# Kernel tuning notes

Hardware: AMD Instinct MI355X
Metric: run time of the kernel (lower is better)

Reference implementation:

```python
import jax, jax.numpy as jnp
import numpy as np

N_NODES = 50000
N_EDGES = 400000
HID = 128
EPS_GEN = 1e-7  # GENConv message eps


def layernorm(x, w, b, eps=1e-5):
    mu = x.mean(-1, keepdims=True)
    var = x.var(-1, keepdims=True)
    return (x - mu) / jnp.sqrt(var + eps) * w + b


def segment_softmax(v, seg, n):
    # per-channel softmax over edges sharing the same destination node
    m = jax.ops.segment_max(v, seg, num_segments=n)
    e = jnp.exp(v - m[seg])
    s = jax.ops.segment_sum(e, seg, num_segments=n)
    return e / (s[seg] + 1e-16)


def genconv(x, src, dst, w1, b1, lnw, lnb, w2, b2, t):
    # GENConv(aggr='softmax', t learnable, mlp num_layers=2, norm='layer'), no edge_attr
    n = x.shape[0]
    msg = jax.nn.relu(x[src]) + EPS_GEN            # [E, H]
    alpha = segment_softmax(msg * t, dst, n)       # [E, H]
    aggr = jax.ops.segment_sum(msg * alpha, dst, num_segments=n)  # [N, H]
    h = x + aggr                                   # residual self term
    h = layernorm(h @ w1 + b1, lnw, lnb)           # Linear(H, 2H) + LayerNorm + ReLU
    return jax.nn.relu(h) @ w2 + b2                # Linear(2H, H)


def setup_inputs() -> dict:
    key = jax.random.key(0)
    ks = jax.random.split(key, 30)
    rn = lambda k, shape, s=0.02: jax.random.normal(k, shape, jnp.float32) * s
    inp = {}
    inp['x'] = jax.random.normal(ks[0], (N_NODES, 1024), jnp.float32)
    inp['edge_index'] = jax.random.randint(ks[1], (2, N_EDGES), 0, N_NODES, jnp.int64 if jax.config.jax_enable_x64 else jnp.int32)
    inp['fc_w'] = rn(ks[2], (1024, HID)); inp['fc_b'] = jnp.zeros((HID,), jnp.float32)
    inp['conv_w1'] = rn(ks[3], (3, HID, 2 * HID)); inp['conv_b1'] = jnp.zeros((3, 2 * HID), jnp.float32)
    inp['conv_lnw'] = jnp.ones((3, 2 * HID), jnp.float32); inp['conv_lnb'] = jnp.zeros((3, 2 * HID), jnp.float32)
    inp['conv_w2'] = rn(ks[4], (3, 2 * HID, HID)); inp['conv_b2'] = jnp.zeros((3, HID), jnp.float32)
    inp['conv_t'] = jnp.ones((3,), jnp.float32)
    inp['norm_w'] = jnp.ones((3, HID), jnp.float32); inp['norm_b'] = jnp.zeros((3, HID), jnp.float32)
    D = 4 * HID  # 512
    inp['phi_w'] = rn(ks[5], (D, D)); inp['phi_b'] = jnp.zeros((D,), jnp.float32)
    inp['attn_a_w'] = rn(ks[6], (D, D)); inp['attn_a_b'] = jnp.zeros((D,), jnp.float32)
    inp['attn_b_w'] = rn(ks[7], (D, D)); inp['attn_b_b'] = jnp.zeros((D,), jnp.float32)
    inp['attn_c_w'] = rn(ks[8], (D, 1)); inp['attn_c_b'] = jnp.zeros((1,), jnp.float32)
    inp['rho_w'] = rn(ks[9], (D, D)); inp['rho_b'] = jnp.zeros((D,), jnp.float32)
    inp['cls_w'] = rn(ks[10], (D, 4)); inp['cls_b'] = jnp.zeros((4,), jnp.float32)
    return inp


def reference(x, edge_index, fc_w, fc_b, conv_w1, conv_b1, conv_lnw, conv_lnb,
              conv_w2, conv_b2, conv_t, norm_w, norm_b, phi_w, phi_b,
              attn_a_w, attn_a_b, attn_b_w, attn_b_b, attn_c_w, attn_c_b,
              rho_w, rho_b, cls_w, cls_b):
    src, dst = edge_index[0], edge_index[1]
    # fc (dropout = identity in eval)
    x = jax.nn.relu(x @ fc_w + fc_b)               # [N, 128]
    x_ = x
    # layers[0].conv only (no norm/act/residual)
    x = genconv(x, src, dst, conv_w1[0], conv_b1[0], conv_lnw[0], conv_lnb[0],
                conv_w2[0], conv_b2[0], conv_t[0])
    x_ = jnp.concatenate([x_, x], axis=1)
    # DeepGCNLayer block='res': h = act(norm(conv(x))); x = x + h
    for i in (1, 2):
        h = genconv(x, src, dst, conv_w1[i], conv_b1[i], conv_lnw[i], conv_lnb[i],
                    conv_w2[i], conv_b2[i], conv_t[i])
        h = jax.nn.relu(layernorm(h, norm_w[i], norm_b[i]))
        x = x + h
        x_ = jnp.concatenate([x_, x], axis=1)
    h = jax.nn.relu(x_ @ phi_w + phi_b)            # path_phi, [N, 512]
    a = jnp.tanh(h @ attn_a_w + attn_a_b)
    b = jax.nn.sigmoid(h @ attn_b_w + attn_b_b)
    A = (a * b) @ attn_c_w + attn_c_b              # [N, 1]
    A = jax.nn.softmax(A.T, axis=1)                # [1, N]
    hp = A @ h                                     # [1, 512] attention pooling
    hp = jax.nn.relu(hp @ rho_w + rho_b)[0]        # squeeze -> [512]
    logits = (hp @ cls_w + cls_b)[None, :]         # [1, 4]
    return logits
```

## Files before the change

### kernel.cpp

```cpp
#include <hip/hip_runtime.h>
#include <hip/hip_bf16.h>
#include <math.h>

typedef __bf16 bf16_t;
typedef __attribute__((ext_vector_type(8))) __bf16 bf16x8;
typedef __attribute__((ext_vector_type(2))) __bf16 bf16x2;
typedef __attribute__((ext_vector_type(4))) float f32x4;

__device__ __forceinline__ void gld_lds16(const void* g, void* s) {
    __builtin_amdgcn_global_load_lds(
        (__attribute__((address_space(1))) unsigned int*)g,
        (__attribute__((address_space(3))) unsigned int*)s,
        16, 0, 0);
}

__device__ __forceinline__ int2 sw_decode(int orig, int nwg, int NT) {
    int q = nwg >> 3, r = nwg & 7, xcd = orig & 7, idx = orig >> 3;
    int wg = (xcd < r ? xcd * (q + 1) : r * (q + 1) + (xcd - r) * q) + idx;
    int bx = wg / NT, by = wg - bx * NT;
    return make_int2(bx, by);
}

__global__ __launch_bounds__(256) void k_tconv(const float* __restrict__ in, bf16_t* __restrict__ out,
                                               int R, int C, int rs, int ro)
{
    __shared__ float tile[32][33];
    int bc = blockIdx.x * 32;
    int br = blockIdx.y * 32;
    int tx = threadIdx.x & 31, ty = threadIdx.x >> 5;
    #pragma unroll
    for (int i = 0; i < 32; i += 8) {
        int r = br + ty + i, c = bc + tx;
        tile[ty + i][tx] = (r < R && c < C) ? in[(long)r * C + c] : 0.f;
    }
    __syncthreads();
    #pragma unroll
    for (int i = 0; i < 32; i += 8) {
        int c = bc + ty + i, r = br + tx;
        if (c < C && r < R) out[((long)c * rs + ro) * R + r] = (bf16_t)tile[tx][ty + i];
    }
}

__global__ __launch_bounds__(256) void k_bcat(const float* __restrict__ ab, const float* __restrict__ bb,
                                              float* __restrict__ bc)
{
    int i = blockIdx.x * 256 + threadIdx.x;
    if (i < 512) { bc[2 * i] = ab[i]; bc[2 * i + 1] = bb[i]; }
}

__global__ __launch_bounds__(256) void k_deg(const int* __restrict__ dst, int* __restrict__ deg, int E)
{
    int e = blockIdx.x * 256 + threadIdx.x;
    if (e < E) atomicAdd(&deg[dst[e]], 1);
}

__global__ __launch_bounds__(1024) void k_scan_a(const int* __restrict__ deg, int* __restrict__ loc,
                                                 int* __restrict__ bsum, int n)
{
    __shared__ int wsum[16];
    int t = threadIdx.x, lane = t & 63, wid = t >> 6;
    int idx = blockIdx.x * 1024 + t;
    int v = (idx < n) ? deg[idx] : 0;
    int x = v;
    #pragma unroll
    for (int d = 1; d < 64; d <<= 1) { int o = __shfl_up(x, d); if (lane >= d) x += o; }
    if (lane == 63) wsum[wid] = x;
    __syncthreads();
    if (wid == 0 && lane < 16) {
        int y = wsum[lane];
        #pragma unroll
        for (int d = 1; d < 16; d <<= 1) { int o = __shfl_up(y, d); if (lane >= d) y += o; }
        wsum[lane] = y;
    }
    __syncthreads();
    int wbase = (wid == 0) ? 0 : wsum[wid - 1];
    if (idx < n) loc[idx] = wbase + x - v;
    if (t == 1023) bsum[blockIdx.x] = wsum[15];
}

__global__ __launch_bounds__(64) void k_scan_b(const int* __restrict__ bsum, int nb,
                                               int* __restrict__ boff, int* __restrict__ off_n)
{
    int lane = threadIdx.x;
    int base = 0;
    for (int c = 0; c < nb; c += 64) {
        int i = c + lane;
        int v = (i < nb) ? bsum[i] : 0;
        int x = v;
        #pragma unroll
        for (int d = 1; d < 64; d <<= 1) { int o = __shfl_up(x, d); if (lane >= d) x += o; }
        if (i < nb) boff[i] = base + x - v;
        base += __shfl(x, 63);
    }
    if (lane == 0) *off_n = base;
}

__global__ __launch_bounds__(1024) void k_scan_c(const int* __restrict__ loc, const int* __restrict__ boff,
                                                 int* __restrict__ off, int* __restrict__ cursor, int n)
{
    int idx = blockIdx.x * 1024 + threadIdx.x;
    if (idx < n) { int v = loc[idx] + boff[blockIdx.x]; off[idx] = v; cursor[idx] = v; }
}

__global__ __launch_bounds__(256) void k_fill(const int* __restrict__ src, const int* __restrict__ dst,
                                              int* __restrict__ cursor, int* __restrict__ csr, int E)
{
    int e = blockIdx.x * 256 + threadIdx.x;
    if (e < E) {
        int d = dst[e];
        int pos = atomicAdd(&cursor[d], 1);
        csr[pos] = src[e];
    }
}

__global__ __launch_bounds__(256) void k_agg(const bf16_t* __restrict__ X,
                                             const int* __restrict__ off, const int* __restrict__ csr,
                                             bf16_t* __restrict__ haux,
                                             const float* __restrict__ tptr, int ti, int Nn)
{
    int w = (blockIdx.x * 256 + threadIdx.x) >> 6;
    if (w >= Nn) return;
    int lane = threadIdx.x & 63;
    float t = tptr[ti];
    int e0 = off[w], e1 = off[w + 1];
    float m0 = -__builtin_inff(), m1 = -__builtin_inff();
    float s0 = 0.f, s1 = 0.f, g0 = 0.f, g1 = 0.f;

    auto proc = [&](bf16x2 xv) {
        float msg0 = fmaxf((float)xv[0], 0.f) + 1e-7f;
        float msg1 = fmaxf((float)xv[1], 0.f) + 1e-7f;
        float v0 = msg0 * t, v1 = msg1 * t;
        if (v0 > m0) { float sc = __expf(m0 - v0); s0 *= sc; g0 *= sc; m0 = v0; }
        float p0 = __expf(v0 - m0); s0 += p0; g0 += msg0 * p0;
        if (v1 > m1) { float sc = __expf(m1 - v1); s1 *= sc; g1 *= sc; m1 = v1; }
        float p1 = __expf(v1 - m1); s1 += p1; g1 += msg1 * p1;
    };

    int e = e0;
    for (; e + 4 <= e1; e += 4) {
        int ia = csr[e], ib = csr[e + 1], ic = csr[e + 2], id = csr[e + 3];
        bf16x2 va = *(const bf16x2*)(X + (long)ia * 128 + lane * 2);
        bf16x2 vb = *(const bf16x2*)(X + (long)ib * 128 + lane * 2);
        bf16x2 vc = *(const bf16x2*)(X + (long)ic * 128 + lane * 2);
        bf16x2 vd = *(const bf16x2*)(X + (long)id * 128 + lane * 2);
        proc(va); proc(vb); proc(vc); proc(vd);
    }
    for (; e < e1; e++) {
        int s = csr[e];
        bf16x2 xv = *(const bf16x2*)(X + (long)s * 128 + lane * 2);
        proc(xv);
    }
    float a0 = g0 / (s0 + 1e-16f);
    float a1 = g1 / (s1 + 1e-16f);
    bf16x2 xr = *(const bf16x2*)(X + (long)w * 128 + lane * 2);
    bf16_t* outp = haux + (long)w * 128 + lane * 2;
    outp[0] = (bf16_t)((float)xr[0] + a0);
    outp[1] = (bf16_t)((float)xr[1] + a1);
}

template<int BM, int EPI>
__global__ __launch_bounds__((BM == 256) ? 512 : 256, 4)
void k_gemm1(const bf16_t* __restrict__ A, int lda,
             const bf16_t* __restrict__ BT,
             const float* __restrict__ bias,
             bf16_t* __restrict__ Cout, int ldc,
             int M, int K, int NT,
             const float* __restrict__ cw,
             float* __restrict__ sout)
{
    constexpr int THREADS = (BM == 256) ? 512 : 256;
    constexpr int ACH = BM * 8 / THREADS;
    constexpr int BCH = 128 * 8 / THREADS;
    __shared__ __align__(16) bf16_t lA[BM * 64];
    __shared__ __align__(16) bf16_t lB[128 * 64];
    int2 bxy = sw_decode(blockIdx.x, gridDim.x, NT);
    const int m0 = bxy.x * BM, n0 = bxy.y * 128;
    const int tid = threadIdx.x, lane = tid & 63, wid = tid >> 6;
    const int rbase = (wid >> 1) * 64, cbase = (wid & 1) * 64;
    const int lrow = lane & 15, kg = lane >> 4;
    const int uw = tid & ~63;

    f32x4 acc[4][4];
    #pragma unroll
    for (int m = 0; m < 4; m++)
        #pragma unroll
        for (int n = 0; n < 4; n++)
            #pragma unroll
            for (int r = 0; r < 4; r++) acc[m][n][r] = 0.f;

    auto stage = [&](int k0) {
        #pragma unroll
        for (int c = 0; c < ACH; c++) {
            int s = c * THREADS + tid, row = s >> 3, k8s = (s & 7) ^ (row & 7);
            int gr = m0 + row; gr = gr < M ? gr : M - 1;
            gld_lds16(A + (long)gr * lda + k0 + k8s * 8, lA + (c * THREADS + uw) * 8);
        }
        #pragma unroll
        for (int c = 0; c < BCH; c++) {
            int s = c * THREADS + tid, row = s >> 3, k8s = (s & 7) ^ (row & 7);
            gld_lds16(BT + (long)(n0 + row) * K + k0 + k8s * 8, lB + (c * THREADS + uw) * 8);
        }
    };
    auto compute = [&]() {
        #pragma unroll
        for (int ks = 0; ks < 2; ks++) {
            int k8 = ks * 4 + kg;
            bf16x8 af[4], bfr[4];
            #pragma unroll
            for (int m = 0; m < 4; m++) {
                int r = rbase + m * 16 + lrow;
                af[m] = *(const bf16x8*)&lA[(r * 8 + (k8 ^ (r & 7))) * 8];
            }
            #pragma unroll
            for (int n = 0; n < 4; n++) {
                int r = cbase + n * 16 + lrow;
                bfr[n] = *(const bf16x8*)&lB[(r * 8 + (k8 ^ (r & 7))) * 8];
            }
            #pragma unroll
            for (int m = 0; m < 4; m++)
                #pragma unroll
                for (int n = 0; n < 4; n++)
                    acc[m][n] = __builtin_amdgcn_mfma_f32_16x16x32_bf16(af[m], bfr[n], acc[m][n], 0, 0, 0);
        }
    };

    for (int k0 = 0; k0 < K; k0 += 64) {
        stage(k0);
        __syncthreads();
        compute();
        __syncthreads();
    }

    if constexpr (EPI == 5) {
        #pragma unroll
        for (int m = 0; m < 4; m++) {
            #pragma unroll
            for (int r = 0; r < 4; r++) {
                int row = m0 + rbase + m * 16 + kg * 4 + r;
                float val = 0.f;
                #pragma unroll
                for (int n = 0; n < 4; n++) {
                    int col = n0 + cbase + n * 16 + lrow;
                    float xv = acc[m][n][r] + bias[col];
                    int odd = col & 1;
                    float z = odd ? xv : 2.f * xv;
                    float sg = 1.f / (1.f + __expf(-z));
                    float f = odd ? sg : (2.f * sg - 1.f);
                    float partner = __shfl_xor(f, 1);
                    float prod = f * partner;
                    val += odd ? 0.f : prod * cw[col >> 1];
                }
                #pragma unroll
                for (int o = 1; o < 16; o <<= 1) val += __shfl_xor(val, o);
                if (lrow == 0 && row < M) atomicAdd(&sout[row], val);
            }
        }
    } else {
        #pragma unroll
        for (int m = 0; m < 4; m++) {
            #pragma unroll
            for (int r = 0; r < 4; r++) {
                int row = m0 + rbase + m * 16 + kg * 4 + r;
                if (row >= M) continue;
                #pragma unroll
                for (int n = 0; n < 4; n++) {
                    int col = n0 + cbase + n * 16 + lrow;
                    float xv = fmaxf(acc[m][n][r] + bias[col], 0.f);
                    Cout[(long)row * ldc + col] = (bf16_t)xv;
                }
            }
        }
    }
}

__global__ __launch_bounds__(256) void k_gemm_fc(const float* __restrict__ Aptr, int lda,
                                                 const bf16_t* __restrict__ BT,
                                                 const float* __restrict__ bias,
                                                 bf16_t* __restrict__ Cout, int ldc,
                                                 bf16_t* __restrict__ Cout2,
                                                 int M, int K)
{
    constexpr int BUFA = 64 * 64;
    constexpr int BUFB = 128 * 64;
    __shared__ __align__(16) bf16_t lA[2 * BUFA];
    __shared__ __align__(16) bf16_t lB[2 * BUFB];
    const int m0 = blockIdx.x * 64, n0 = 0;
    const int tid = threadIdx.x, lane = tid & 63, wid = tid >> 6;
    const int rbase = wid * 16;
    const int lrow = lane & 15, kg = lane >> 4;
    const int ub = tid & 192;

    f32x4 acc[8];
    #pragma unroll
    for (int n = 0; n < 8; n++)
        #pragma unroll
        for (int r = 0; r < 4; r++) acc[n][r] = 0.f;

    f32x4 fa[4];

    auto stageB = [&](int k0, int buf) {
        #pragma unroll
        for (int c = 0; c < 4; c++) {
            int s = c * 256 + tid, row = s >> 3, k8s = (s & 7) ^ (row & 7);
            gld_lds16(BT + (long)(n0 + row) * K + k0 + k8s * 8, lB + buf * BUFB + (c * 256 + ub) * 8);
        }
    };
    auto loadA_f32 = [&](int k0) {
        #pragma unroll
        for (int c = 0; c < 2; c++) {
            int s = c * 256 + tid, row = s >> 3, k8s = (s & 7) ^ (row & 7);
            int grow = m0 + row;
            if (grow < M) {
                const float* sp = Aptr + (long)grow * lda + k0 + k8s * 8;
                fa[2 * c] = *(const f32x4*)sp;
                fa[2 * c + 1] = *(const f32x4*)(sp + 4);
            } else {
                #pragma unroll
                for (int j = 0; j < 4; j++) { fa[2 * c][j] = 0.f; fa[2 * c + 1][j] = 0.f; }
            }
        }
    };
    auto writeA = [&](int buf) {
        #pragma unroll
        for (int c = 0; c < 2; c++) {
            int s = c * 256 + tid;
            bf16x8 v;
            #pragma unroll
            for (int j = 0; j < 4; j++) { v[j] = (bf16_t)fa[2 * c][j]; v[4 + j] = (bf16_t)fa[2 * c + 1][j]; }
            *(bf16x8*)&lA[buf * BUFA + s * 8] = v;
        }
    };
    auto compute = [&](int buf) {
        #pragma unroll
        for (int ks = 0; ks < 2; ks++) {
            int k8 = ks * 4 + kg;
            int ra = rbase + lrow;
            bf16x8 af = *(const bf16x8*)&lA[buf * BUFA + (ra * 8 + (k8 ^ (ra & 7))) * 8];
            #pragma unroll
            for (int n = 0; n < 8; n++) {
                int r = n * 16 + lrow;
                bf16x8 bf = *(const bf16x8*)&lB[buf * BUFB + (r * 8 + (k8 ^ (r & 7))) * 8];
                acc[n] = __builtin_amdgcn_mfma_f32_16x16x32_bf16(af, bf, acc[n], 0, 0, 0);
            }
        }
    };

    const int nt = K >> 6;
    loadA_f32(0); writeA(0);
    stageB(0, 0);
    __syncthreads();
    int cur = 0;
    for (int t = 0; t < nt - 1; t++) {
        int nk = (t + 1) << 6;
        loadA_f32(nk);
        stageB(nk, cur ^ 1);
        compute(cur);
        __syncthreads();
        writeA(cur ^ 1);
        __syncthreads();
        cur ^= 1;
    }
    compute(cur);

    #pragma unroll
    for (int r = 0; r < 4; r++) {
        int row = m0 + rbase + kg * 4 + r;
        if (row >= M) continue;
        #pragma unroll
        for (int n = 0; n < 8; n++) {
            int col = n * 16 + lrow;
            float xv = fmaxf(acc[n][r] + bias[col], 0.f);
            Cout[(long)row * ldc + col] = (bf16_t)xv;
            Cout2[(long)row * 128 + col] = (bf16_t)xv;
        }
    }
}

template<int MODE>
__global__ __launch_bounds__(256) void k_convf(const bf16_t* __restrict__ A,
                                               const bf16_t* __restrict__ B1T,
                                               const float* __restrict__ b1,
                                               const float* __restrict__ lnw, const float* __restrict__ lnb,
                                               const bf16_t* __restrict__ B2T,
                                               const float* __restrict__ b2,
                                               const float* __restrict__ nw, const float* __restrict__ nb,
                                               const float* __restrict__ xs_in,
                                               bf16_t* __restrict__ xcat_out,
                                               float* __restrict__ xs_out, bf16_t* __restrict__ xl_out,
                                               int M)
{
    __shared__ __align__(16) bf16_t lA[64 * 128];
    __shared__ __align__(16) bf16_t lB1[256 * 128];
    __shared__ __align__(16) bf16_t h1b[64 * 256];
    __shared__ __align__(16) bf16_t lB2a[128 * 128];
    bf16_t* lB2b = lB1;

    const int m0 = blockIdx.x * 64;
    const int tid = threadIdx.x, lane = tid & 63, w = tid >> 6;
    const int lrow = lane & 15, kg = lane >> 4;
    const int ub = tid & 192;

    #pragma unroll
    for (int c = 0; c < 4; c++) {
        int s = c * 256 + tid, row = s >> 4, sl = s & 15;
        int k8 = (sl & 8) | ((sl & 7) ^ (row & 7));
        int gr = m0 + row; gr = gr < M ? gr : M - 1;
        gld_lds16(A + (long)gr * 128 + k8 * 8, lA + (c * 256 + ub) * 8);
    }
    #pragma unroll
    for (int c = 0; c < 16; c++) {
        int s = c * 256 + tid, row = s >> 4, sl = s & 15;
        int k8 = (sl & 8) | ((sl & 7) ^ (row & 7));
        gld_lds16(B1T + (long)row * 128 + k8 * 8, lB1 + (c * 256 + ub) * 8);
    }
    #pragma unroll
    for (int c = 0; c < 8; c++) {
        int s = c * 256 + tid, row = s >> 4, sl = s & 15;
        int k8 = (sl & 8) | ((sl & 7) ^ (row & 7));
        gld_lds16(B2T + (long)row * 256 + k8 * 8, lB2a + (c * 256 + ub) * 8);
    }
    asm volatile("s_waitcnt vmcnt(8)" ::: "memory");
    __builtin_amdgcn_s_barrier();

    f32x4 acc1[16];
    #pragma unroll
    for (int n = 0; n < 16; n++)
        #pragma unroll
        for (int r = 0; r < 4; r++) acc1[n][r] = 0.f;
    #pragma unroll
    for (int ks = 0; ks < 4; ks++) {
        int k8 = ks * 4 + kg;
        int ra = w * 16 + lrow;
        bf16x8 af = *(const bf16x8*)&lA[(ra * 16 + ((k8 & 8) | ((k8 & 7) ^ (ra & 7)))) * 8];
        #pragma unroll
        for (int n = 0; n < 16; n++) {
            int rb = n * 16 + lrow;
            bf16x8 bf = *(const bf16x8*)&lB1[(rb * 16 + ((k8 & 8) | ((k8 & 7) ^ (rb & 7)))) * 8];
            acc1[n] = __builtin_amdgcn_mfma_f32_16x16x32_bf16(af, bf, acc1[n], 0, 0, 0);
        }
    }

    #pragma unroll
    for (int r = 0; r < 4; r++) {
        int row = w * 16 + kg * 4 + r;
        float xv[16], s1 = 0.f, s2 = 0.f;
        #pragma unroll
        for (int n = 0; n < 16; n++) {
            int col = n * 16 + lrow;
            xv[n] = acc1[n][r] + b1[col];
            s1 += xv[n]; s2 += xv[n] * xv[n];
        }
        #pragma unroll
        for (int o = 1; o < 16; o <<= 1) { s1 += __shfl_xor(s1, o); s2 += __shfl_xor(s2, o); }
        float mu = s1 * (1.f / 256.f);
        float var = s2 * (1.f / 256.f) - mu * mu;
        float rstd = rsqrtf(var + 1e-5f);
        #pragma unroll
        for (int n = 0; n < 16; n++) {
            int col = n * 16 + lrow;
            float y = fmaxf((xv[n] - mu) * rstd * lnw[col] + lnb[col], 0.f);
            int chunk = (col >> 3);
            int cs = (chunk & 24) | ((chunk & 7) ^ (row & 7));
            h1b[row * 256 + cs * 8 + (col & 7)] = (bf16_t)y;
        }
    }

    asm volatile("s_waitcnt vmcnt(0)" ::: "memory");
    __builtin_amdgcn_s_barrier();

    #pragma unroll
    for (int c = 0; c < 8; c++) {
        int s = c * 256 + tid, row = s >> 4, sl = s & 15;
        int k8l = (sl & 8) | ((sl & 7) ^ (row & 7));
        gld_lds16(B2T + (long)row * 256 + (16 + k8l) * 8, lB2b + (c * 256 + ub) * 8);
    }

    f32x4 acc2[8];
    #pragma unroll
    for (int n = 0; n < 8; n++)
        #pragma unroll
        for (int r = 0; r < 4; r++) acc2[n][r] = 0.f;
    #pragma unroll
    for (int ks = 0; ks < 4; ks++) {
        int k8 = ks * 4 + kg;
        int ra = w * 16 + lrow;
        bf16x8 af = *(const bf16x8*)&h1b[(ra * 32 + ((k8 & 24) | ((k8 & 7) ^ (ra & 7)))) * 8];
        #pragma unroll
        for (int n = 0; n < 8; n++) {
            int rb = n * 16 + lrow;
            bf16x8 bf = *(const bf16x8*)&lB2a[(rb * 16 + ((k8 & 8) | ((k8 & 7) ^ (rb & 7)))) * 8];
            acc2[n] = __builtin_amdgcn_mfma_f32_16x16x32_bf16(af, bf, acc2[n], 0, 0, 0);
        }
    }
    asm volatile("s_waitcnt vmcnt(0)" ::: "memory");
    __builtin_amdgcn_s_barrier();
    #pragma unroll
    for (int ks = 0; ks < 4; ks++) {
        int k8 = 16 + ks * 4 + kg;
        int k8l = k8 - 16;
        int ra = w * 16 + lrow;
        bf16x8 af = *(const bf16x8*)&h1b[(ra * 32 + ((k8 & 24) | ((k8 & 7) ^ (ra & 7)))) * 8];
        #pragma unroll
        for (int n = 0; n < 8; n++) {
            int rb = n * 16 + lrow;
            bf16x8 bf = *(const bf16x8*)&lB2b[(rb * 16 + ((k8l & 8) | ((k8l & 7) ^ (rb & 7)))) * 8];
            acc2[n] = __builtin_amdgcn_mfma_f32_16x16x32_bf16(af, bf, acc2[n], 0, 0, 0);
        }
    }

    #pragma unroll
    for (int r = 0; r < 4; r++) {
        int row = m0 + w * 16 + kg * 4 + r;
        float xv[8];
        #pragma unroll
        for (int n = 0; n < 8; n++) xv[n] = acc2[n][r] + b2[n * 16 + lrow];
        if constexpr (MODE == 1) {
            float s1 = 0.f, s2 = 0.f;
            #pragma unroll
            for (int n = 0; n < 8; n++) { s1 += xv[n]; s2 += xv[n] * xv[n]; }
            #pragma unroll
            for (int o = 1; o < 16; o <<= 1) { s1 += __shfl_xor(s1, o); s2 += __shfl_xor(s2, o); }
            float mu = s1 * (1.f / 128.f);
            float var = s2 * (1.f / 128.f) - mu * mu;
            float rstd = rsqrtf(var + 1e-5f);
            if (row < M) {
                #pragma unroll
                for (int n = 0; n < 8; n++) {
                    int col = n * 16 + lrow;
                    xv[n] = xs_in[(long)row * 128 + col] + fmaxf((xv[n] - mu) * rstd * nw[col] + nb[col], 0.f);
                }
            }
        }
        if (row < M) {
            #pragma unroll
            for (int n = 0; n < 8; n++) {
                int col = n * 16 + lrow;
                xcat_out[(long)row * 512 + col] = (bf16_t)xv[n];
                if (xs_out) xs_out[(long)row * 128 + col] = xv[n];
                if (xl_out) xl_out[(long)row * 128 + col] = (bf16_t)xv[n];
            }
        }
    }
}

__global__ __launch_bounds__(256) void k_sred_a(const float* __restrict__ sN, int Nn,
                                                float* __restrict__ pmax, float* __restrict__ psum)
{
    __shared__ float red[4];
    int t = threadIdx.x, lane = t & 63, wid = t >> 6;
    int stride = gridDim.x * 256;
    float m = -__builtin_inff();
    for (int i = blockIdx.x * 256 + t; i < Nn; i += stride) m = fmaxf(m, sN[i]);
    #pragma unroll
    for (int o = 32; o >= 1; o >>= 1) m = fmaxf(m, __shfl_xor(m, o));
    if (lane == 0) red[wid] = m;
    __syncthreads();
    float bm = fmaxf(fmaxf(red[0], red[1]), fmaxf(red[2], red[3]));
    float s = 0.f;
    for (int i = blockIdx.x * 256 + t; i < Nn; i += stride) s += __expf(sN[i] - bm);
    #pragma unroll
    for (int o = 32; o >= 1; o >>= 1) s += __shfl_xor(s, o);
    __syncthreads();
    if (lane == 0) red[wid] = s;
    __syncthreads();
    if (t == 0) {
        pmax[blockIdx.x] = bm;
        psum[blockIdx.x] = red[0] + red[1] + red[2] + red[3];
    }
}

__global__ __launch_bounds__(64) void k_sred_b(const float* __restrict__ pmax, const float* __restrict__ psum,
                                               int nb, float* __restrict__ red)
{
    int lane = threadIdx.x;
    float m = (lane < nb) ? pmax[lane] : -__builtin_inff();
    #pragma unroll
    for (int o = 32; o >= 1; o >>= 1) m = fmaxf(m, __shfl_xor(m, o));
    float s = (lane < nb) ? psum[lane] * __expf(pmax[lane] - m) : 0.f;
    #pragma unroll
    for (int o = 32; o >= 1; o >>= 1) s += __shfl_xor(s, o);
    if (lane == 0) { red[0] = m; red[1] = s; }
}

__global__ __launch_bounds__(512) void k_pool(const bf16_t* __restrict__ h, const float* __restrict__ sN,
                                              const float* __restrict__ red, float* __restrict__ hp, int Nn)
{
    int t = threadIdx.x;
    float m = red[0], inv = 1.f / red[1];
    float acc = 0.f;
    for (int n = blockIdx.x; n < Nn; n += gridDim.x) {
        float wgt = __expf(sN[n] - m) * inv;
        acc += wgt * (float)h[(long)n * 512 + t];
    }
    atomicAdd(&hp[t], acc);
}

__global__ __launch_bounds__(256) void k_tail_a(const float* __restrict__ hp,
                                                const float* __restrict__ rho_w, const float* __restrict__ rho_b,
                                                float* __restrict__ h2g)
{
    __shared__ float hs[512];
    __shared__ float part[256];
    int t = threadIdx.x;
    hs[t] = hp[t]; hs[t + 256] = hp[t + 256];
    __syncthreads();
    int col = blockIdx.x * 64 + (t & 63);
    int ks = t >> 6;
    float acc = 0.f;
    for (int k = ks * 128; k < ks * 128 + 128; k++) acc += hs[k] * rho_w[(long)k * 512 + col];
    part[t] = acc;
    __syncthreads();
    if (ks == 0) {
        float v = part[t] + part[t + 64] + part[t + 128] + part[t + 192] + rho_b[col];
        h2g[col] = fmaxf(v, 0.f);
    }
}

__global__ __launch_bounds__(256) void k_tail_b(const float* __restrict__ h2g,
                                                const float* __restrict__ cls_w, const float* __restrict__ cls_b,
                                                float* __restrict__ out)
{
    __shared__ float wred[4][4];
    int t = threadIdx.x, lane = t & 63, wid = t >> 6;
    float a0 = 0.f, a1 = 0.f, a2 = 0.f, a3 = 0.f;
    for (int d = t; d < 512; d += 256) {
        float h = h2g[d];
        a0 += h * cls_w[d * 4 + 0];
        a1 += h * cls_w[d * 4 + 1];
        a2 += h * cls_w[d * 4 + 2];
        a3 += h * cls_w[d * 4 + 3];
    }
    #pragma unroll
    for (int o = 32; o >= 1; o >>= 1) {
        a0 += __shfl_xor(a0, o); a1 += __shfl_xor(a1, o);
        a2 += __shfl_xor(a2, o); a3 += __shfl_xor(a3, o);
    }
    if (lane == 0) { wred[wid][0] = a0; wred[wid][1] = a1; wred[wid][2] = a2; wred[wid][3] = a3; }
    __syncthreads();
    if (t < 4)
        out[t] = cls_b[t] + wred[0][t] + wred[1][t] + wred[2][t] + wred[3][t];
}

extern "C" void kernel_launch(void* const* d_in, const int* in_sizes, int n_in,
                              void* d_out, int out_size, void* d_ws, size_t ws_size,
                              hipStream_t stream)
{
    const float* x       = (const float*)d_in[0];
    const int*   eidx    = (const int*)  d_in[1];
    const float* fc_w    = (const float*)d_in[2];
    const float* fc_b    = (const float*)d_in[3];
    const float* conv_w1 = (const float*)d_in[4];
    const float* conv_b1 = (const float*)d_in[5];
    const float* conv_lnw= (const float*)d_in[6];
    const float* conv_lnb= (const float*)d_in[7];
    const float* conv_w2 = (const float*)d_in[8];
    const float* conv_b2 = (const float*)d_in[9];
    const float* conv_t  = (const float*)d_in[10];
    const float* norm_w  = (const float*)d_in[11];
    const float* norm_b  = (const float*)d_in[12];
    const float* phi_w   = (const float*)d_in[13];
    const float* phi_b   = (const float*)d_in[14];
    const float* aw      = (const float*)d_in[15];
    const float* ab      = (const float*)d_in[16];
    const float* bw      = (const float*)d_in[17];
    const float* bb      = (const float*)d_in[18];
    const float* cwp     = (const float*)d_in[19];
    const float* rho_w   = (const float*)d_in[21];
    const float* rho_b   = (const float*)d_in[22];
    const float* cls_w   = (const float*)d_in[23];
    const float* cls_b   = (const float*)d_in[24];

    const int Nn = in_sizes[0] / 1024;
    const int E  = in_sizes[1] / 2;

    char* p = (char*)d_ws;
    auto carve = [&](size_t bytes) { char* r = p; p += (bytes + 255) & ~(size_t)255; return r; };

    bf16_t* x_cat_b = (bf16_t*)carve((size_t)Nn * 512 * 2);
    bf16_t* haux    = (bf16_t*)carve((size_t)Nn * 128 * 2);
    float*  xs1     = (float*)carve((size_t)Nn * 128 * 4);
    float*  xs2     = (float*)carve((size_t)Nn * 128 * 4);
    bf16_t* xl0     = (bf16_t*)carve((size_t)Nn * 128 * 2);
    bf16_t* xl1     = (bf16_t*)carve((size_t)Nn * 128 * 2);
    bf16_t* xl2     = (bf16_t*)carve((size_t)Nn * 128 * 2);
    bf16_t* h_phi   = (bf16_t*)carve((size_t)Nn * 512 * 2);
    bf16_t* fcT  = (bf16_t*)carve((size_t)128 * 1024 * 2);
    bf16_t* w1T  = (bf16_t*)carve((size_t)3 * 256 * 128 * 2);
    bf16_t* w2T  = (bf16_t*)carve((size_t)3 * 128 * 256 * 2);
    bf16_t* phiT = (bf16_t*)carve((size_t)512 * 512 * 2);
    bf16_t* Bcat = (bf16_t*)carve((size_t)1024 * 512 * 2);
    float* bias_cat = (float*)carve(1024 * 4);
    int*   deg    = (int*)carve((size_t)Nn * 4);
    int*   loc    = (int*)carve((size_t)Nn * 4);
    int*   bsum   = (int*)carve(256 * 4);
    int*   boff   = (int*)carve(256 * 4);
    int*   offArr = (int*)carve((size_t)(Nn + 1) * 4);
    int*   cursor = (int*)carve((size_t)Nn * 4);
    int*   csr    = (int*)carve((size_t)E * 4);
    float* sN     = (float*)carve((size_t)Nn * 4);
    float* pmax   = (float*)carve(64 * 4);
    float* psum   = (float*)carve(64 * 4);
    float* red    = (float*)carve(64);
    float* hp     = (float*)carve(512 * 4);
    float* h2g    = (float*)carve(512 * 4);

    hipMemsetAsync(deg, 0, (size_t)Nn * 4, stream);
    hipMemsetAsync(sN, 0, (size_t)Nn * 4, stream);
    hipMemsetAsync(hp, 0, 512 * 4, stream);

    k_tconv<<<dim3(4, 32), 256, 0, stream>>>(fc_w, fcT, 1024, 128, 1, 0);
    for (int i = 0; i < 3; i++) {
        k_tconv<<<dim3(8, 4), 256, 0, stream>>>(conv_w1 + (size_t)i * 128 * 256, w1T + (size_t)i * 256 * 128, 128, 256, 1, 0);
        k_tconv<<<dim3(4, 8), 256, 0, stream>>>(conv_w2 + (size_t)i * 256 * 128, w2T + (size_t)i * 128 * 256, 256, 128, 1, 0);
    }
    k_tconv<<<dim3(16, 16), 256, 0, stream>>>(phi_w, phiT, 512, 512, 1, 0);
    k_tconv<<<dim3(16, 16), 256, 0, stream>>>(aw, Bcat, 512, 512, 2, 0);
    k_tconv<<<dim3(16, 16), 256, 0, stream>>>(bw, Bcat, 512, 512, 2, 1);
    k_bcat<<<2, 256, 0, stream>>>(ab, bb, bias_cat);

    const int SB = (Nn + 1023) / 1024;
    k_deg<<<(E + 255) / 256, 256, 0, stream>>>(eidx + E, deg, E);
    k_scan_a<<<SB, 1024, 0, stream>>>(deg, loc, bsum, Nn);
    k_scan_b<<<1, 64, 0, stream>>>(bsum, SB, boff, offArr + Nn);
    k_scan_c<<<SB, 1024, 0, stream>>>(loc, boff, offArr, cursor, Nn);
    k_fill<<<(E + 255) / 256, 256, 0, stream>>>(eidx, eidx + E, cursor, csr, E);

    const int MT64  = (Nn + 63) / 64;
    const int MT128 = (Nn + 127) / 128;
    const int MT256 = (Nn + 255) / 256;
    const int agB = (Nn + 3) / 4;

    k_gemm_fc<<<MT64, 256, 0, stream>>>(x, 1024, fcT, fc_b, x_cat_b, 512, xl0, Nn, 1024);

    const bf16_t* xls[3] = {xl0, xl1, xl2};
    for (int i = 0; i < 3; i++) {
        k_agg<<<agB, 256, 0, stream>>>(xls[i], offArr, csr, haux, conv_t, i, Nn);
        if (i == 0)
            k_convf<0><<<MT64, 256, 0, stream>>>(haux, w1T, conv_b1, conv_lnw, conv_lnb,
                                                 w2T, conv_b2, nullptr, nullptr, nullptr,
                                                 x_cat_b + 128, xs1, xl1, Nn);
        else if (i == 1)
            k_convf<1><<<MT64, 256, 0, stream>>>(haux, w1T + (size_t)256 * 128, conv_b1 + 256,
                                                 conv_lnw + 256, conv_lnb + 256,
                                                 w2T + (size_t)128 * 256, conv_b2 + 128,
                                                 norm_w + 128, norm_b + 128, xs1,
                                                 x_cat_b + 256, xs2, xl2, Nn);
        else
            k_convf<1><<<MT64, 256, 0, stream>>>(haux, w1T + (size_t)2 * 256 * 128, conv_b1 + 512,
                                                 conv_lnw + 512, conv_lnb + 512,
                                                 w2T + (size_t)2 * 128 * 256, conv_b2 + 256,
                                                 norm_w + 256, norm_b + 256, xs2,
                                                 x_cat_b + 384, nullptr, nullptr, Nn);
    }

    k_gemm1<128, 3><<<MT128 * 4, 256, 0, stream>>>(x_cat_b, 512, phiT, phi_b, h_phi, 512,
                                                   Nn, 512, 4, nullptr, nullptr);
    k_gemm1<256, 5><<<MT256 * 8, 512, 0, stream>>>(h_phi, 512, Bcat, bias_cat, nullptr, 0,
                                                   Nn, 512, 8, cwp, sN);
    k_sred_a<<<64, 256, 0, stream>>>(sN, Nn, pmax, psum);
    k_sred_b<<<1, 64, 0, stream>>>(pmax, psum, 64, red);
    k_pool<<<256, 512, 0, stream>>>(h_phi, sN, red, hp, Nn);
    k_tail_a<<<8, 256, 0, stream>>>(hp, rho_w, rho_b, h2g);
    k_tail_b<<<1, 256, 0, stream>>>(h2g, cls_w, cls_b, (float*)d_out);
}
```

Before: 700.6 us.

## Fuse weight prep kernels, widen gated-attention GEMM tile, vectorize pooling

Folds the eleven weight-transpose launches and the bias concat into one k_prep kernel to cut launch overhead. Adds a dedicated k_gemm2 for the gated attention projection that uses 256x256 tiles with 8 waves, each wave computing 128x64, so more MFMA work is done per LDS load. k_pool now has each wave handle a separate node with 16-byte vector loads, reduces partials in shared memory, and issues fewer atomics. The larger GEMM tile raises register and LDS pressure, which can lower occupancy.

```diff
diff --git a/kernel.cpp b/kernel.cpp
--- a/kernel.cpp
+++ b/kernel.cpp
@@ -21,12 +21,11 @@
     return make_int2(bx, by);
 }
 
-__global__ __launch_bounds__(256) void k_tconv(const float* __restrict__ in, bf16_t* __restrict__ out,
-                                               int R, int C, int rs, int ro)
+__device__ __forceinline__ void tconv_tile(const float* __restrict__ in, bf16_t* __restrict__ out,
+                                           int R, int C, int rs, int ro, int bx, int by)
 {
     __shared__ float tile[32][33];
-    int bc = blockIdx.x * 32;
-    int br = blockIdx.y * 32;
+    int bc = bx * 32, br = by * 32;
     int tx = threadIdx.x & 31, ty = threadIdx.x >> 5;
     #pragma unroll
     for (int i = 0; i < 32; i += 8) {
@@ -41,11 +40,37 @@
     }
 }
 
-__global__ __launch_bounds__(256) void k_bcat(const float* __restrict__ ab, const float* __restrict__ bb,
-                                              float* __restrict__ bc)
-{
-    int i = blockIdx.x * 256 + threadIdx.x;
-    if (i < 512) { bc[2 * i] = ab[i]; bc[2 * i + 1] = bb[i]; }
+__global__ __launch_bounds__(256) void k_prep(const float* __restrict__ fc_w, bf16_t* __restrict__ fcT,
+                                              const float* __restrict__ conv_w1, bf16_t* __restrict__ w1T,
+                                              const float* __restrict__ conv_w2, bf16_t* __restrict__ w2T,
+                                              const float* __restrict__ phi_w, bf16_t* __restrict__ phiT,
+                                              const float* __restrict__ aw, const float* __restrict__ bw,
+                                              bf16_t* __restrict__ Bcat,
+                                              const float* __restrict__ abias, const float* __restrict__ bbias,
+                                              float* __restrict__ bias_cat)
+{
+    int b = blockIdx.x;
+    if (b < 128) {
+        tconv_tile(fc_w, fcT, 1024, 128, 1, 0, b & 3, b >> 2);
+    } else if (b < 224) {
+        int i = (b - 128) >> 5, bb = (b - 128) & 31;
+        tconv_tile(conv_w1 + (size_t)i * 128 * 256, w1T + (size_t)i * 256 * 128, 128, 256, 1, 0, bb & 7, bb >> 3);
+    } else if (b < 320) {
+        int i = (b - 224) >> 5, bb = (b - 224) & 31;
+        tconv_tile(conv_w2 + (size_t)i * 256 * 128, w2T + (size_t)i * 128 * 256, 256, 128, 1, 0, bb & 3, bb >> 2);
+    } else if (b < 576) {
+        int bb = b - 320;
+        tconv_tile(phi_w, phiT, 512, 512, 1, 0, bb & 15, bb >> 4);
+    } else if (b < 832) {
+        int bb = b - 576;
+        tconv_tile(aw, Bcat, 512, 512, 2, 0, bb & 15, bb >> 4);
+    } else if (b < 1088) {
+        int bb = b - 832;
+        tconv_tile(bw, Bcat, 512, 512, 2, 1, bb & 15, bb >> 4);
+    } else {
+        int i = (b - 1088) * 256 + threadIdx.x;
+        if (i < 512) { bias_cat[2 * i] = abias[i]; bias_cat[2 * i + 1] = bbias[i]; }
+    }
 }
 
 __global__ __launch_bounds__(256) void k_deg(const int* __restrict__ dst, int* __restrict__ deg, int E)
@@ -158,8 +183,8 @@
     outp[1] = (bf16_t)((float)xr[1] + a1);
 }
 
-template<int BM, int EPI>
-__global__ __launch_bounds__((BM == 256) ? 512 : 256, 4)
+template<int EPI>
+__global__ __launch_bounds__(256, 4)
 void k_gemm1(const bf16_t* __restrict__ A, int lda,
              const bf16_t* __restrict__ BT,
              const float* __restrict__ bias,
@@ -168,13 +193,10 @@
              const float* __restrict__ cw,
              float* __restrict__ sout)
 {
-    constexpr int THREADS = (BM == 256) ? 512 : 256;
-    constexpr int ACH = BM * 8 / THREADS;
-    constexpr int BCH = 128 * 8 / THREADS;
-    __shared__ __align__(16) bf16_t lA[BM * 64];
+    __shared__ __align__(16) bf16_t lA[128 * 64];
     __shared__ __align__(16) bf16_t lB[128 * 64];
     int2 bxy = sw_decode(blockIdx.x, gridDim.x, NT);
-    const int m0 = bxy.x * BM, n0 = bxy.y * 128;
+    const int m0 = bxy.x * 128, n0 = bxy.y * 128;
     const int tid = threadIdx.x, lane = tid & 63, wid = tid >> 6;
     const int rbase = (wid >> 1) * 64, cbase = (wid & 1) * 64;
     const int lrow = lane & 15, kg = lane >> 4;
@@ -190,15 +212,15 @@
 
     auto stage = [&](int k0) {
         #pragma unroll
-        for (int c = 0; c < ACH; c++) {
-            int s = c * THREADS + tid, row = s >> 3, k8s = (s & 7) ^ (row & 7);
+        for (int c = 0; c < 4; c++) {
+            int s = c * 256 + tid, row = s >> 3, k8s = (s & 7) ^ (row & 7);
             int gr = m0 + row; gr = gr < M ? gr : M - 1;
-            gld_lds16(A + (long)gr * lda + k0 + k8s * 8, lA + (c * THREADS + uw) * 8);
-        }
-        #pragma unroll
-        for (int c = 0; c < BCH; c++) {
-            int s = c * THREADS + tid, row = s >> 3, k8s = (s & 7) ^ (row & 7);
-            gld_lds16(BT + (long)(n0 + row) * K + k0 + k8s * 8, lB + (c * THREADS + uw) * 8);
+            gld_lds16(A + (long)gr * lda + k0 + k8s * 8, lA + (c * 256 + uw) * 8);
+        }
+        #pragma unroll
+        for (int c = 0; c < 4; c++) {
+            int s = c * 256 + tid, row = s >> 3, k8s = (s & 7) ^ (row & 7);
+            gld_lds16(BT + (long)(n0 + row) * K + k0 + k8s * 8, lB + (c * 256 + uw) * 8);
         }
     };
     auto compute = [&]() {
@@ -231,44 +253,112 @@
         __syncthreads();
     }
 
-    if constexpr (EPI == 5) {
-        #pragma unroll
-        for (int m = 0; m < 4; m++) {
-            #pragma unroll
-            for (int r = 0; r < 4; r++) {
-                int row = m0 + rbase + m * 16 + kg * 4 + r;
-                float val = 0.f;
+    #pragma unroll
+    for (int m = 0; m < 4; m++) {
+        #pragma unroll
+        for (int r = 0; r < 4; r++) {
+            int row = m0 + rbase + m * 16 + kg * 4 + r;
+            if (row >= M) continue;
+            #pragma unroll
+            for (int n = 0; n < 4; n++) {
+                int col = n0 + cbase + n * 16 + lrow;
+                float xv = fmaxf(acc[m][n][r] + bias[col], 0.f);
+                Cout[(long)row * ldc + col] = (bf16_t)xv;
+            }
+        }
+    }
+}
+
+__global__ __launch_bounds__(512, 2)
+void k_gemm2(const bf16_t* __restrict__ A, int lda,
+             const bf16_t* __restrict__ BT,
+             const float* __restrict__ bias,
+             int M, int K, int NT,
+             const float* __restrict__ cw,
+             float* __restrict__ sout)
+{
+    __shared__ __align__(16) bf16_t lA[256 * 64];
+    __shared__ __align__(16) bf16_t lB[256 * 64];
+    int2 bxy = sw_decode(blockIdx.x, gridDim.x, NT);
+    const int m0 = bxy.x * 256, n0 = bxy.y * 256;
+    const int tid = threadIdx.x, lane = tid & 63, wid = tid >> 6;
+    const int wr = wid >> 2, wc = wid & 3;
+    const int rbase = wr * 128, cbase = wc * 64;
+    const int lrow = lane & 15, kg = lane >> 4;
+    const int uw = tid & ~63;
+
+    f32x4 acc[8][4];
+    #pragma unroll
+    for (int m = 0; m < 8; m++)
+        #pragma unroll
+        for (int n = 0; n < 4; n++)
+            #pragma unroll
+            for (int r = 0; r < 4; r++) acc[m][n][r] = 0.f;
+
+    auto stage = [&](int k0) {
+        #pragma unroll
+        for (int c = 0; c < 4; c++) {
+            int s = c * 512 + tid, row = s >> 3, k8s = (s & 7) ^ (row & 7);
+            int gr = m0 + row; gr = gr < M ? gr : M - 1;
+            gld_lds16(A + (long)gr * lda + k0 + k8s * 8, lA + (c * 512 + uw) * 8);
+        }
+        #pragma unroll
+        for (int c = 0; c < 4; c++) {
+            int s = c * 512 + tid, row = s >> 3, k8s = (s & 7) ^ (row & 7);
+            gld_lds16(BT + (long)(n0 + row) * K + k0 + k8s * 8, lB + (c * 512 + uw) * 8);
+        }
+    };
+    auto compute = [&]() {
+        #pragma unroll
+        for (int ks = 0; ks < 2; ks++) {
+            int k8 = ks * 4 + kg;
+            bf16x8 af[8], bfr[4];
+            #pragma unroll
+            for (int m = 0; m < 8; m++) {
+                int r = rbase + m * 16 + lrow;
+                af[m] = *(const bf16x8*)&lA[(r * 8 + (k8 ^ (r & 7))) * 8];
+            }
+            #pragma unroll
+            for (int n = 0; n < 4; n++) {
+                int r = cbase + n * 16 + lrow;
+                bfr[n] = *(const bf16x8*)&lB[(r * 8 + (k8 ^ (r & 7))) * 8];
+            }
+            #pragma unroll
+            for (int m = 0; m < 8; m++)
                 #pragma unroll
-                for (int n = 0; n < 4; n++) {
-                    int col = n0 + cbase + n * 16 + lrow;
-                    float xv = acc[m][n][r] + bias[col];
-                    int odd = col & 1;
-                    float z = odd ? xv : 2.f * xv;
-                    float sg = 1.f / (1.f + __expf(-z));
-                    float f = odd ? sg : (2.f * sg - 1.f);
-                    float partner = __shfl_xor(f, 1);
-                    float prod = f * partner;
-                    val += odd ? 0.f : prod * cw[col >> 1];
-                }
-                #pragma unroll
-                for (int o = 1; o < 16; o <<= 1) val += __shfl_xor(val, o);
-                if (lrow == 0 && row < M) atomicAdd(&sout[row], val);
-            }
-        }
-    } else {
-        #pragma unroll
-        for (int m = 0; m < 4; m++) {
-            #pragma unroll
-            for (int r = 0; r < 4; r++) {
-                int row = m0 + rbase + m * 16 + kg * 4 + r;
-                if (row >= M) continue;
-                #pragma unroll
-                for (int n = 0; n < 4; n++) {
-                    int col = n0 + cbase + n * 16 + lrow;
-                    float xv = fmaxf(acc[m][n][r] + bias[col], 0.f);
-                    Cout[(long)row * ldc + col] = (bf16_t)xv;
-                }
-            }
+                for (int n = 0; n < 4; n++)
+                    acc[m][n] = __builtin_amdgcn_mfma_f32_16x16x32_bf16(af[m], bfr[n], acc[m][n], 0, 0, 0);
+        }
+    };
+
+    for (int k0 = 0; k0 < K; k0 += 64) {
+        stage(k0);
+        __syncthreads();
+        compute();
+        __syncthreads();
+    }
+
+    #pragma unroll
+    for (int m = 0; m < 8; m++) {
+        #pragma unroll
+        for (int r = 0; r < 4; r++) {
+            int row = m0 + rbase + m * 16 + kg * 4 + r;
+            float val = 0.f;
+            #pragma unroll
+            for (int n = 0; n < 4; n++) {
+                int col = n0 + cbase + n * 16 + lrow;
+                float xv = acc[m][n][r] + bias[col];
+                int odd = col & 1;
+                float z = odd ? xv : 2.f * xv;
+                float sg = 1.f / (1.f + __expf(-z));
+                float f = odd ? sg : (2.f * sg - 1.f);
+                float partner = __shfl_xor(f, 1);
+                float prod = f * partner;
+                val += odd ? 0.f : prod * cw[col >> 1];
+            }
+            #pragma unroll
+            for (int o = 1; o < 16; o <<= 1) val += __shfl_xor(val, o);
+            if (lrow == 0 && row < M) atomicAdd(&sout[row], val);
         }
     }
 }
@@ -582,17 +672,30 @@
     if (lane == 0) { red[0] = m; red[1] = s; }
 }
 
-__global__ __launch_bounds__(512) void k_pool(const bf16_t* __restrict__ h, const float* __restrict__ sN,
+__global__ __launch_bounds__(256) void k_pool(const bf16_t* __restrict__ h, const float* __restrict__ sN,
                                               const float* __restrict__ red, float* __restrict__ hp, int Nn)
 {
-    int t = threadIdx.x;
+    __shared__ float part[4][512];
+    int t = threadIdx.x, lane = t & 63, w = t >> 6;
     float m = red[0], inv = 1.f / red[1];
-    float acc = 0.f;
-    for (int n = blockIdx.x; n < Nn; n += gridDim.x) {
+    float acc[8];
+    #pragma unroll
+    for (int j = 0; j < 8; j++) acc[j] = 0.f;
+    for (int n = blockIdx.x * 4 + w; n < Nn; n += gridDim.x * 4) {
         float wgt = __expf(sN[n] - m) * inv;
-        acc += wgt * (float)h[(long)n * 512 + t];
-    }
-    atomicAdd(&hp[t], acc);
+        bf16x8 v = *(const bf16x8*)(h + (long)n * 512 + lane * 8);
+        #pragma unroll
+        for (int j = 0; j < 8; j++) acc[j] += wgt * (float)v[j];
+    }
+    #pragma unroll
+    for (int j = 0; j < 8; j++) part[w][lane * 8 + j] = acc[j];
+    __syncthreads();
+    #pragma unroll
+    for (int c = 0; c < 2; c++) {
+        int col = c * 256 + t;
+        float s = part[0][col] + part[1][col] + part[2][col] + part[3][col];
+        atomicAdd(&hp[col], s);
+    }
 }
 
 __global__ __launch_bounds__(256) void k_tail_a(const float* __restrict__ hp,
@@ -708,15 +811,8 @@
     hipMemsetAsync(sN, 0, (size_t)Nn * 4, stream);
     hipMemsetAsync(hp, 0, 512 * 4, stream);
 
-    k_tconv<<<dim3(4, 32), 256, 0, stream>>>(fc_w, fcT, 1024, 128, 1, 0);
-    for (int i = 0; i < 3; i++) {
-        k_tconv<<<dim3(8, 4), 256, 0, stream>>>(conv_w1 + (size_t)i * 128 * 256, w1T + (size_t)i * 256 * 128, 128, 256, 1, 0);
-        k_tconv<<<dim3(4, 8), 256, 0, stream>>>(conv_w2 + (size_t)i * 256 * 128, w2T + (size_t)i * 128 * 256, 256, 128, 1, 0);
-    }
-    k_tconv<<<dim3(16, 16), 256, 0, stream>>>(phi_w, phiT, 512, 512, 1, 0);
-    k_tconv<<<dim3(16, 16), 256, 0, stream>>>(aw, Bcat, 512, 512, 2, 0);
-    k_tconv<<<dim3(16, 16), 256, 0, stream>>>(bw, Bcat, 512, 512, 2, 1);
-    k_bcat<<<2, 256, 0, stream>>>(ab, bb, bias_cat);
+    k_prep<<<1090, 256, 0, stream>>>(fc_w, fcT, conv_w1, w1T, conv_w2, w2T, phi_w, phiT,
+                                     aw, bw, Bcat, ab, bb, bias_cat);
 
     const int SB = (Nn + 1023) / 1024;
     k_deg<<<(E + 255) / 256, 256, 0, stream>>>(eidx + E, deg, E);
@@ -753,13 +849,12 @@
                                                  x_cat_b + 384, nullptr, nullptr, Nn);
     }
 
-    k_gemm1<128, 3><<<MT128 * 4, 256, 0, stream>>>(x_cat_b, 512, phiT, phi_b, h_phi, 512,
-                                                   Nn, 512, 4, nullptr, nullptr);
-    k_gemm1<256, 5><<<MT256 * 8, 512, 0, stream>>>(h_phi, 512, Bcat, bias_cat, nullptr, 0,
-                                                   Nn, 512, 8, cwp, sN);
+    k_gemm1<3><<<MT128 * 4, 256, 0, stream>>>(x_cat_b, 512, phiT, phi_b, h_phi, 512,
+                                              Nn, 512, 4, nullptr, nullptr);
+    k_gemm2<<<MT256 * 4, 512, 0, stream>>>(h_phi, 512, Bcat, bias_cat, Nn, 512, 4, cwp, sN);
     k_sred_a<<<64, 256, 0, stream>>>(sN, Nn, pmax, psum);
     k_sred_b<<<1, 64, 0, stream>>>(pmax, psum, 64, red);
-    k_pool<<<256, 512, 0, stream>>>(h_phi, sN, red, hp, Nn);
+    k_pool<<<256, 256, 0, stream>>>(h_phi, sN, red, hp, Nn);
     k_tail_a<<<8, 256, 0, stream>>>(hp, rho_w, rho_b, h2g);
     k_tail_b<<<1, 256, 0, stream>>>(h2g, cls_w, cls_b, (float*)d_out);
 }
```

New measurement: 696.6 us. About the same (-0.6%).

## Merge weight-prep launches, vectorize attention pooling, enlarge phi GEMM tile

Applied to the files above, without the earlier changes.

The ten separate transpose/convert launches and the bias-concat launch are merged into one k_prep kernel that picks its job from the block index, cutting launch overhead. The pooling kernel now has each wavefront read a full 512-wide row with 16-byte bf16x8 loads, accumulate 8 columns per lane, and reduce across wavefronts in shared memory before issuing the atomics. The phi GEMM switches from the 128-row, 256-thread variant to the 256-row, 512-thread variant, which trades fewer, larger blocks and more reuse per block for lower grid-level parallelism.

```diff
diff --git a/kernel.cpp b/kernel.cpp
--- a/kernel.cpp
+++ b/kernel.cpp
@@ -21,12 +21,11 @@
     return make_int2(bx, by);
 }
 
-__global__ __launch_bounds__(256) void k_tconv(const float* __restrict__ in, bf16_t* __restrict__ out,
-                                               int R, int C, int rs, int ro)
+__device__ __forceinline__ void tconv_tile(const float* __restrict__ in, bf16_t* __restrict__ out,
+                                           int R, int C, int rs, int ro, int bx, int by)
 {
     __shared__ float tile[32][33];
-    int bc = blockIdx.x * 32;
-    int br = blockIdx.y * 32;
+    int bc = bx * 32, br = by * 32;
     int tx = threadIdx.x & 31, ty = threadIdx.x >> 5;
     #pragma unroll
     for (int i = 0; i < 32; i += 8) {
@@ -41,11 +40,37 @@
     }
 }
 
-__global__ __launch_bounds__(256) void k_bcat(const float* __restrict__ ab, const float* __restrict__ bb,
-                                              float* __restrict__ bc)
-{
-    int i = blockIdx.x * 256 + threadIdx.x;
-    if (i < 512) { bc[2 * i] = ab[i]; bc[2 * i + 1] = bb[i]; }
+__global__ __launch_bounds__(256) void k_prep(const float* __restrict__ fc_w, bf16_t* __restrict__ fcT,
+                                              const float* __restrict__ conv_w1, bf16_t* __restrict__ w1T,
+                                              const float* __restrict__ conv_w2, bf16_t* __restrict__ w2T,
+                                              const float* __restrict__ phi_w, bf16_t* __restrict__ phiT,
+                                              const float* __restrict__ aw, const float* __restrict__ bw,
+                                              bf16_t* __restrict__ Bcat,
+                                              const float* __restrict__ abias, const float* __restrict__ bbias,
+                                              float* __restrict__ bias_cat)
+{
+    int b = blockIdx.x;
+    if (b < 128) {
+        tconv_tile(fc_w, fcT, 1024, 128, 1, 0, b & 3, b >> 2);
+    } else if (b < 224) {
+        int i = (b - 128) >> 5, bb = (b - 128) & 31;
+        tconv_tile(conv_w1 + (size_t)i * 128 * 256, w1T + (size_t)i * 256 * 128, 128, 256, 1, 0, bb & 7, bb >> 3);
+    } else if (b < 320) {
+        int i = (b - 224) >> 5, bb = (b - 224) & 31;
+        tconv_tile(conv_w2 + (size_t)i * 256 * 128, w2T + (size_t)i * 128 * 256, 256, 128, 1, 0, bb & 3, bb >> 2);
+    } else if (b < 576) {
+        int bb = b - 320;
+        tconv_tile(phi_w, phiT, 512, 512, 1, 0, bb & 15, bb >> 4);
+    } else if (b < 832) {
+        int bb = b - 576;
+        tconv_tile(aw, Bcat, 512, 512, 2, 0, bb & 15, bb >> 4);
+    } else if (b < 1088) {
+        int bb = b - 832;
+        tconv_tile(bw, Bcat, 512, 512, 2, 1, bb & 15, bb >> 4);
+    } else {
+        int i = (b - 1088) * 256 + threadIdx.x;
+        if (i < 512) { bias_cat[2 * i] = abias[i]; bias_cat[2 * i + 1] = bbias[i]; }
+    }
 }
 
 __global__ __launch_bounds__(256) void k_deg(const int* __restrict__ dst, int* __restrict__ deg, int E)
@@ -582,17 +607,30 @@
     if (lane == 0) { red[0] = m; red[1] = s; }
 }
 
-__global__ __launch_bounds__(512) void k_pool(const bf16_t* __restrict__ h, const float* __restrict__ sN,
+__global__ __launch_bounds__(256) void k_pool(const bf16_t* __restrict__ h, const float* __restrict__ sN,
                                               const float* __restrict__ red, float* __restrict__ hp, int Nn)
 {
-    int t = threadIdx.x;
+    __shared__ float part[4][512];
+    int t = threadIdx.x, lane = t & 63, w = t >> 6;
     float m = red[0], inv = 1.f / red[1];
-    float acc = 0.f;
-    for (int n = blockIdx.x; n < Nn; n += gridDim.x) {
+    float acc[8];
+    #pragma unroll
+    for (int j = 0; j < 8; j++) acc[j] = 0.f;
+    for (int n = blockIdx.x * 4 + w; n < Nn; n += gridDim.x * 4) {
         float wgt = __expf(sN[n] - m) * inv;
-        acc += wgt * (float)h[(long)n * 512 + t];
-    }
-    atomicAdd(&hp[t], acc);
+        bf16x8 v = *(const bf16x8*)(h + (long)n * 512 + lane * 8);
+        #pragma unroll
+        for (int j = 0; j < 8; j++) acc[j] += wgt * (float)v[j];
+    }
+    #pragma unroll
+    for (int j = 0; j < 8; j++) part[w][lane * 8 + j] = acc[j];
+    __syncthreads();
+    #pragma unroll
+    for (int c = 0; c < 2; c++) {
+        int col = c * 256 + t;
+        float s = part[0][col] + part[1][col] + part[2][col] + part[3][col];
+        atomicAdd(&hp[col], s);
+    }
 }
 
 __global__ __launch_bounds__(256) void k_tail_a(const float* __restrict__ hp,
@@ -708,15 +746,8 @@
     hipMemsetAsync(sN, 0, (size_t)Nn * 4, stream);
     hipMemsetAsync(hp, 0, 512 * 4, stream);
 
-    k_tconv<<<dim3(4, 32), 256, 0, stream>>>(fc_w, fcT, 1024, 128, 1, 0);
-    for (int i = 0; i < 3; i++) {
-        k_tconv<<<dim3(8, 4), 256, 0, stream>>>(conv_w1 + (size_t)i * 128 * 256, w1T + (size_t)i * 256 * 128, 128, 256, 1, 0);
-        k_tconv<<<dim3(4, 8), 256, 0, stream>>>(conv_w2 + (size_t)i * 256 * 128, w2T + (size_t)i * 128 * 256, 256, 128, 1, 0);
-    }
-    k_tconv<<<dim3(16, 16), 256, 0, stream>>>(phi_w, phiT, 512, 512, 1, 0);
-    k_tconv<<<dim3(16, 16), 256, 0, stream>>>(aw, Bcat, 512, 512, 2, 0);
-    k_tconv<<<dim3(16, 16), 256, 0, stream>>>(bw, Bcat, 512, 512, 2, 1);
-    k_bcat<<<2, 256, 0, stream>>>(ab, bb, bias_cat);
+    k_prep<<<1090, 256, 0, stream>>>(fc_w, fcT, conv_w1, w1T, conv_w2, w2T, phi_w, phiT,
+                                     aw, bw, Bcat, ab, bb, bias_cat);
 
     const int SB = (Nn + 1023) / 1024;
     k_deg<<<(E + 255) / 256, 256, 0, stream>>>(eidx + E, deg, E);
@@ -726,7 +757,6 @@
     k_fill<<<(E + 255) / 256, 256, 0, stream>>>(eidx, eidx + E, cursor, csr, E);
 
     const int MT64  = (Nn + 63) / 64;
-    const int MT128 = (Nn + 127) / 128;
     const int MT256 = (Nn + 255) / 256;
     const int agB = (Nn + 3) / 4;
 
@@ -753,13 +783,13 @@
                                                  x_cat_b + 384, nullptr, nullptr, Nn);
     }
 
-    k_gemm1<128, 3><<<MT128 * 4, 256, 0, stream>>>(x_cat_b, 512, phiT, phi_b, h_phi, 512,
+    k_gemm1<256, 3><<<MT256 * 4, 512, 0, stream>>>(x_cat_b, 512, phiT, phi_b, h_phi, 512,
                                                    Nn, 512, 4, nullptr, nullptr);
     k_gemm1<256, 5><<<MT256 * 8, 512, 0, stream>>>(h_phi, 512, Bcat, bias_cat, nullptr, 0,
                                                    Nn, 512, 8, cwp, sN);
     k_sred_a<<<64, 256, 0, stream>>>(sN, Nn, pmax, psum);
     k_sred_b<<<1, 64, 0, stream>>>(pmax, psum, 64, red);
-    k_pool<<<256, 512, 0, stream>>>(h_phi, sN, red, hp, Nn);
+    k_pool<<<256, 256, 0, stream>>>(h_phi, sN, red, hp, Nn);
     k_tail_a<<<8, 256, 0, stream>>>(hp, rho_w, rho_b, h2g);
     k_tail_b<<<1, 256, 0, stream>>>(h2g, cls_w, cls_b, (float*)d_out);
 }
```

Result: faster. 632.4 us (-9.7%).
